# Optimization experiments

Hardware: AMD Instinct MI355X
Metric: run time of the kernel (lower is better)

## Reference

```python
import jax, jax.numpy as jnp
import numpy as np

B = 128          # batch of codewords
M_CHK = 288      # n_check_nodes
N_VAR = 576      # n_variable_nodes
K_INFO = 288     # n_information_bits
N_ITER = 5
EDGE_P = 0.02    # ~11-12 edges per check row, LDPC-like sparsity


def setup_inputs() -> dict:
    key = jax.random.key(0)
    k1, k2, k3, k4 = jax.random.split(key, 4)
    inputs = jax.random.normal(k1, (B, N_VAR), dtype=jnp.float32)
    # sparse binary parity-check matrix, batched (keras RNN constants carry batch dim)
    H = jax.random.bernoulli(k2, EDGE_P, (B, M_CHK, N_VAR)).astype(jnp.float32)
    sigma2 = 0.5 + 0.5 * jax.random.uniform(k3, (B, 1), dtype=jnp.float32)
    # learned parameters
    input_ponderation = jnp.ones((N_ITER, 1), dtype=jnp.float32)
    out_ponderation = jnp.ones((N_ITER, 1), dtype=jnp.float32)
    skip_ponderation = jnp.ones((1, 1), dtype=jnp.float32)
    # per-edge check-to-variable weights of the neural BP cell
    w_cv = 1.0 + 0.02 * jax.random.normal(k4, (M_CHK, N_VAR), dtype=jnp.float32)
    gate_logit = jnp.asarray(0.0, dtype=jnp.float32)
    return {"inputs": inputs, "H": H, "sigma2": sigma2,
            "input_ponderation": input_ponderation,
            "out_ponderation": out_ponderation,
            "skip_ponderation": skip_ponderation,
            "w_cv": w_cv, "gate_logit": gate_logit}


def _decode(inputs, H, sigma2, input_ponderation, out_ponderation,
            skip_ponderation, w_cv, gate_logit):
    llrs = -4.0 * inputs / sigma2                                    # [B, n]
    # trainable=True path: normalize by mean |llr|
    norm_llrs = llrs / jnp.mean(jnp.abs(llrs), axis=-1, keepdims=True)
    # tile over iterations and apply input ponderation -> [B, T, n]
    x = norm_llrs[:, None, :] * input_ponderation

    mask = H                                                         # [B, m, n]
    gate = jax.nn.sigmoid(gate_logit)

    def cell(Mstate, x_t):
        # variable-to-check extrinsic messages on edges
        S = jnp.sum(Mstate, axis=1, keepdims=True)                   # [B, 1, n]
        V = (x_t[:, None, :] + S - Mstate) * mask                    # [B, m, n]
        # tanh-product check-node update (product excluding self via divide)
        t = jnp.tanh(0.5 * jnp.clip(V, -15.0, 15.0))
        t_edge = jnp.where(mask > 0, t, 1.0)
        P = jnp.prod(t_edge, axis=-1, keepdims=True)                 # [B, m, 1]
        t_safe = jnp.where(jnp.abs(t_edge) < 1e-7,
                           jnp.where(t_edge >= 0, 1e-7, -1e-7), t_edge)
        r = jnp.clip(P / t_safe, -1.0 + 1e-6, 1.0 - 1e-6)
        M_new = 2.0 * jnp.arctanh(r) * w_cv * mask                   # weighted c2v
        # gated (damped) state update
        M_out = gate * M_new + (1.0 - gate) * Mstate
        posterior = x_t + jnp.sum(M_out, axis=1)                     # [B, n]
        return M_out, posterior

    M0 = jnp.zeros_like(H)
    xs = jnp.swapaxes(x, 0, 1)                                       # [T, B, n]
    _, posts = jax.lax.scan(cell, M0, xs)
    outputs = jnp.swapaxes(posts, 0, 1)                              # [B, T, n]

    # post-normalization per iteration, weighted pooling over iterations
    norm_out = outputs / jnp.mean(jnp.abs(outputs), axis=-1, keepdims=True)
    pooled = jnp.mean(out_ponderation * norm_out, axis=-2)           # [B, n]
    out = pooled + skip_ponderation * norm_llrs                      # [1,1] broadcast
    return jax.nn.sigmoid(-out[:, :K_INFO])


def reference(inputs, H, sigma2, input_ponderation, out_ponderation,
              skip_ponderation, w_cv, gate_logit):
    return _decode(inputs, H, sigma2, input_ponderation, out_ponderation,
                   skip_ponderation, w_cv, gate_logit)
```

## Files before the change

kernel.cpp:

```cpp
#include <hip/hip_runtime.h>
#include <hip/hip_bf16.h>

#define B_SZ 128
#define MCHK 288
#define NVAR 576
#define KINFO 288
#define NITER 5
#define CAP 40
#define LCAP 3712
#define TPB 1024

__global__ __launch_bounds__(256) void build_edges(const float* __restrict__ H,
                                                   int* __restrict__ cntG,
                                                   unsigned short* __restrict__ idxG) {
    int row  = blockIdx.x * 4 + (threadIdx.x >> 6);
    int lane = threadIdx.x & 63;
    const float* hrow = H + (size_t)row * NVAR;
    const float4* h4  = (const float4*)hrow;
    float4 a = h4[lane];
    float4 bq = h4[64 + lane];
    float  c = hrow[512 + lane];
    int cnt = (a.x!=0.f)+(a.y!=0.f)+(a.z!=0.f)+(a.w!=0.f)
            + (bq.x!=0.f)+(bq.y!=0.f)+(bq.z!=0.f)+(bq.w!=0.f) + (c!=0.f);
    int pre = cnt;
    #pragma unroll
    for (int o = 1; o < 64; o <<= 1) {
        int n = __shfl_up(pre, o, 64);
        if (lane >= o) pre += n;
    }
    int p = pre - cnt;
    unsigned short* dst = idxG + (size_t)row * CAP;
    int base = lane * 4;
    if (a.x!=0.f)  { if (p<CAP) dst[p] = (unsigned short)(base    ); p++; }
    if (a.y!=0.f)  { if (p<CAP) dst[p] = (unsigned short)(base + 1); p++; }
    if (a.z!=0.f)  { if (p<CAP) dst[p] = (unsigned short)(base + 2); p++; }
    if (a.w!=0.f)  { if (p<CAP) dst[p] = (unsigned short)(base + 3); p++; }
    if (bq.x!=0.f) { if (p<CAP) dst[p] = (unsigned short)(256 + base    ); p++; }
    if (bq.y!=0.f) { if (p<CAP) dst[p] = (unsigned short)(256 + base + 1); p++; }
    if (bq.z!=0.f) { if (p<CAP) dst[p] = (unsigned short)(256 + base + 2); p++; }
    if (bq.w!=0.f) { if (p<CAP) dst[p] = (unsigned short)(256 + base + 3); p++; }
    if (c!=0.f)    { if (p<CAP) dst[p] = (unsigned short)(512 + lane);     p++; }
    if (lane == 63) cntG[row] = (pre > CAP) ? CAP : pre;
}

__global__ __launch_bounds__(TPB) void decode(
    const float* __restrict__ inp,   const float* __restrict__ sigma2,
    const float* __restrict__ ipond, const float* __restrict__ opond,
    const float* __restrict__ skipp, const float* __restrict__ wcv,
    const float* __restrict__ gatel, const int* __restrict__ cntG,
    const unsigned short* __restrict__ idxG, float* __restrict__ out) {

    __shared__ float xln[NVAR];
    __shared__ float S[NVAR];
    __shared__ float pooled[NVAR];
    __shared__ float Prow[MCHK];
    __shared__ float Mld[LCAP];
    __shared__ float tld[LCAP];
    __shared__ unsigned int ev[LCAP];
    __shared__ int   rcnt[MCHK];
    __shared__ int   roff[MCHK];
    __shared__ float red[16];
    __shared__ float scal;
    __shared__ int   EtotS;

    const int b    = blockIdx.x;
    const int tid  = threadIdx.x;
    const int wid  = tid >> 6;
    const int lane = tid & 63;

    const float sig  = sigma2[b];
    const float gate = 1.0f / (1.0f + __expf(-gatel[0]));
    const float gbar = 1.0f - gate;
    const float skip = skipp[0];

    float l = 0.0f, al = 0.0f;
    if (tid < NVAR) { l = -4.0f * inp[(size_t)b * NVAR + tid] / sig; al = fabsf(l); }
    #pragma unroll
    for (int o = 32; o; o >>= 1) al += __shfl_down(al, o, 64);
    if (lane == 0) red[wid] = al;

    int* sc = (int*)tld;
    if (tid < 512) {
        int cc = 0;
        if (tid < MCHK) { cc = cntG[b * MCHK + tid]; rcnt[tid] = cc; }
        sc[tid] = cc;
    }
    __syncthreads();
    if (tid == 0) {
        float s = 0.0f;
        #pragma unroll
        for (int i = 0; i < 16; ++i) s += red[i];
        scal = (float)NVAR / s;
    }
    __syncthreads();
    if (tid < NVAR) {
        xln[tid]    = l * scal;
        pooled[tid] = 0.0f;
        S[tid]      = 0.0f;
    }
    for (int d = 1; d < 512; d <<= 1) {
        int v = 0;
        if (tid < 512) v = sc[tid] + ((tid >= d) ? sc[tid - d] : 0);
        __syncthreads();
        if (tid < 512) sc[tid] = v;
        __syncthreads();
    }
    if (tid < MCHK) {
        int c = rcnt[tid];
        int o = sc[tid] - c;
        if (o >= LCAP)            { o = 0; c = 0; }
        else if (o + c > LCAP)    { c = LCAP - o; }
        roff[tid] = o; rcnt[tid] = c;
        const unsigned short* ig = idxG + ((size_t)b * MCHK + tid) * CAP;
        for (int j = 0; j < c; ++j) {
            int v = ig[j];
            ev[o + j]  = ((unsigned)tid << 16) | (unsigned)v;
            Mld[o + j] = 0.0f;
        }
    }
    if (tid == 0) EtotS = (sc[MCHK - 1] > LCAP) ? LCAP : sc[MCHK - 1];
    __syncthreads();
    const int E = EtotS;

    float ipl[NITER], opl[NITER];
    #pragma unroll
    for (int t = 0; t < NITER; ++t) { ipl[t] = ipond[t]; opl[t] = opond[t]; }

    for (int t = 0; t < NITER; ++t) {
        const float pt = ipl[t], ot = opl[t];

        for (int e = tid; e < E; e += TPB) {
            int v   = (int)(ev[e] & 0xFFFFu);
            float V = fmaf(pt, xln[v], S[v]) - Mld[e];
            V = fminf(15.0f, fmaxf(-15.0f, V));
            float ex = __expf(V);
            float te = (ex - 1.0f) * __builtin_amdgcn_rcpf(ex + 1.0f);
            float x  = 0.5f * V, x2 = x * x;
            float tp = x * fmaf(x2, fmaf(x2, fmaf(x2, -0.05396825f, 0.13333333f),
                                         -0.33333333f), 1.0f);
            tld[e] = (fabsf(V) < 0.5f) ? tp : te;
        }
        __syncthreads();

        if (tid < MCHK) {
            int c = rcnt[tid], o = roff[tid];
            float P = 1.0f;
            for (int j = 0; j < c; ++j) P *= tld[o + j];
            Prow[tid] = P;
        }
        if (tid < NVAR) S[tid] = 0.0f;
        __syncthreads();

        for (int e = tid; e < E; e += TPB) {
            unsigned pk = ev[e];
            int v = (int)(pk & 0xFFFFu);
            int m = (int)(pk >> 16);
            float tj = tld[e];
            float ts = (fabsf(tj) < 1e-7f) ? ((tj >= 0.0f) ? 1e-7f : -1e-7f) : tj;
            float r  = Prow[m] * __builtin_amdgcn_rcpf(ts);
            r = fminf(1.0f - 1e-6f, fmaxf(-1.0f + 1e-6f, r));
            float w  = wcv[m * NVAR + v];
            float Mn = __logf((1.0f + r) * __builtin_amdgcn_rcpf(1.0f - r)) * w;
            float Mo = fmaf(gate, Mn, gbar * Mld[e]);
            Mld[e] = Mo;
            atomicAdd(&S[v], Mo);
        }
        __syncthreads();

        float post = 0.0f, ap = 0.0f;
        if (tid < NVAR) { post = fmaf(pt, xln[tid], S[tid]); ap = fabsf(post); }
        #pragma unroll
        for (int o = 32; o; o >>= 1) ap += __shfl_down(ap, o, 64);
        if (lane == 0) red[wid] = ap;
        __syncthreads();
        if (tid == 0) {
            float s2 = 0.0f;
            #pragma unroll
            for (int i = 0; i < 16; ++i) s2 += red[i];
            scal = (float)NVAR / s2;
        }
        __syncthreads();
        if (tid < NVAR) pooled[tid] += ot * post * scal;
    }

    if (tid < KINFO) {
        float o = pooled[tid] * (1.0f / NITER) + skip * xln[tid];
        out[(size_t)b * KINFO + tid] = 1.0f / (1.0f + __expf(o));
    }
}

extern "C" void kernel_launch(void* const* d_in, const int* in_sizes, int n_in,
                              void* d_out, int out_size, void* d_ws, size_t ws_size,
                              hipStream_t stream) {
    const float* inp    = (const float*)d_in[0];
    const float* H      = (const float*)d_in[1];
    const float* sigma2 = (const float*)d_in[2];
    const float* ipond  = (const float*)d_in[3];
    const float* opond  = (const float*)d_in[4];
    const float* skipp  = (const float*)d_in[5];
    const float* wcv    = (const float*)d_in[6];
    const float* gatel  = (const float*)d_in[7];
    float* out = (float*)d_out;

    int* cntG = (int*)d_ws;
    unsigned short* idxG =
        (unsigned short*)((char*)d_ws + (size_t)B_SZ * MCHK * sizeof(int));

    build_edges<<<(B_SZ * MCHK) / 4, 256, 0, stream>>>(H, cntG, idxG);
    decode<<<B_SZ, TPB, 0, stream>>>(inp, sigma2, ipond, opond, skipp,
                                     wcv, gatel, cntG, idxG, out);
}
```

Measured before the change: 173.7 us.

## Fuse edge-list construction into decode kernel with shared-memory staging

Removes the separate build_edges kernel and has each decode block scan its own batch's H rows, staging per-row edge indices in shared memory that is aliased onto the message/tanh buffers. The block-wide Hillis-Steele row-offset scan with many barriers is replaced by a wave-level shuffle scan plus a small cross-wave sum. This drops one launch and the global round trip of the index lists. In exchange, each of the 128 blocks now streams its 663 KB of H itself, so only 128 blocks share the H read bandwidth instead of many small blocks.

```diff
diff --git a/kernel.cpp b/kernel.cpp
--- a/kernel.cpp
+++ b/kernel.cpp
@@ -1,5 +1,4 @@
 #include <hip/hip_runtime.h>
-#include <hip/hip_bf16.h>
 
 #define B_SZ 128
 #define MCHK 288
@@ -10,58 +9,29 @@
 #define LCAP 3712
 #define TPB 1024
 
-__global__ __launch_bounds__(256) void build_edges(const float* __restrict__ H,
-                                                   int* __restrict__ cntG,
-                                                   unsigned short* __restrict__ idxG) {
-    int row  = blockIdx.x * 4 + (threadIdx.x >> 6);
-    int lane = threadIdx.x & 63;
-    const float* hrow = H + (size_t)row * NVAR;
-    const float4* h4  = (const float4*)hrow;
-    float4 a = h4[lane];
-    float4 bq = h4[64 + lane];
-    float  c = hrow[512 + lane];
-    int cnt = (a.x!=0.f)+(a.y!=0.f)+(a.z!=0.f)+(a.w!=0.f)
-            + (bq.x!=0.f)+(bq.y!=0.f)+(bq.z!=0.f)+(bq.w!=0.f) + (c!=0.f);
-    int pre = cnt;
-    #pragma unroll
-    for (int o = 1; o < 64; o <<= 1) {
-        int n = __shfl_up(pre, o, 64);
-        if (lane >= o) pre += n;
-    }
-    int p = pre - cnt;
-    unsigned short* dst = idxG + (size_t)row * CAP;
-    int base = lane * 4;
-    if (a.x!=0.f)  { if (p<CAP) dst[p] = (unsigned short)(base    ); p++; }
-    if (a.y!=0.f)  { if (p<CAP) dst[p] = (unsigned short)(base + 1); p++; }
-    if (a.z!=0.f)  { if (p<CAP) dst[p] = (unsigned short)(base + 2); p++; }
-    if (a.w!=0.f)  { if (p<CAP) dst[p] = (unsigned short)(base + 3); p++; }
-    if (bq.x!=0.f) { if (p<CAP) dst[p] = (unsigned short)(256 + base    ); p++; }
-    if (bq.y!=0.f) { if (p<CAP) dst[p] = (unsigned short)(256 + base + 1); p++; }
-    if (bq.z!=0.f) { if (p<CAP) dst[p] = (unsigned short)(256 + base + 2); p++; }
-    if (bq.w!=0.f) { if (p<CAP) dst[p] = (unsigned short)(256 + base + 3); p++; }
-    if (c!=0.f)    { if (p<CAP) dst[p] = (unsigned short)(512 + lane);     p++; }
-    if (lane == 63) cntG[row] = (pre > CAP) ? CAP : pre;
-}
-
 __global__ __launch_bounds__(TPB) void decode(
-    const float* __restrict__ inp,   const float* __restrict__ sigma2,
+    const float* __restrict__ inp,   const float* __restrict__ H,
+    const float* __restrict__ sigma2,
     const float* __restrict__ ipond, const float* __restrict__ opond,
     const float* __restrict__ skipp, const float* __restrict__ wcv,
-    const float* __restrict__ gatel, const int* __restrict__ cntG,
-    const unsigned short* __restrict__ idxG, float* __restrict__ out) {
-
+    const float* __restrict__ gatel, float* __restrict__ out) {
+
+    __shared__ __align__(16) float MT[2 * LCAP];
+    __shared__ unsigned int ev[LCAP];
     __shared__ float xln[NVAR];
     __shared__ float S[NVAR];
     __shared__ float pooled[NVAR];
     __shared__ float Prow[MCHK];
-    __shared__ float Mld[LCAP];
-    __shared__ float tld[LCAP];
-    __shared__ unsigned int ev[LCAP];
     __shared__ int   rcnt[MCHK];
     __shared__ int   roff[MCHK];
     __shared__ float red[16];
+    __shared__ int   wsumI[16];
     __shared__ float scal;
     __shared__ int   EtotS;
+
+    float* const Mld = MT;
+    float* const tld = MT + LCAP;
+    unsigned short* const stage = (unsigned short*)MT;
 
     const int b    = blockIdx.x;
     const int tid  = threadIdx.x;
@@ -73,18 +43,77 @@
     const float gbar = 1.0f - gate;
     const float skip = skipp[0];
 
-    float l = 0.0f, al = 0.0f;
-    if (tid < NVAR) { l = -4.0f * inp[(size_t)b * NVAR + tid] / sig; al = fabsf(l); }
+    float l = 0.0f;
+    if (tid < NVAR) l = -4.0f * inp[(size_t)b * NVAR + tid] / sig;
+
+    const float* Hb = H + (size_t)b * (MCHK * NVAR);
+    for (int m = wid; m < MCHK; m += 16) {
+        const float* hrow = Hb + (size_t)m * NVAR;
+        const float4* h4  = (const float4*)hrow;
+        float4 a  = h4[lane];
+        float4 bq = h4[64 + lane];
+        float  c  = hrow[512 + lane];
+        int cnt = (a.x!=0.f)+(a.y!=0.f)+(a.z!=0.f)+(a.w!=0.f)
+                + (bq.x!=0.f)+(bq.y!=0.f)+(bq.z!=0.f)+(bq.w!=0.f) + (c!=0.f);
+        int pre = cnt;
+        #pragma unroll
+        for (int o = 1; o < 64; o <<= 1) {
+            int n = __shfl_up(pre, o, 64);
+            if (lane >= o) pre += n;
+        }
+        int p = pre - cnt;
+        unsigned short* dst = stage + m * CAP;
+        int base = lane * 4;
+        if (a.x!=0.f)  { if (p<CAP) dst[p] = (unsigned short)(base    ); p++; }
+        if (a.y!=0.f)  { if (p<CAP) dst[p] = (unsigned short)(base + 1); p++; }
+        if (a.z!=0.f)  { if (p<CAP) dst[p] = (unsigned short)(base + 2); p++; }
+        if (a.w!=0.f)  { if (p<CAP) dst[p] = (unsigned short)(base + 3); p++; }
+        if (bq.x!=0.f) { if (p<CAP) dst[p] = (unsigned short)(256 + base    ); p++; }
+        if (bq.y!=0.f) { if (p<CAP) dst[p] = (unsigned short)(256 + base + 1); p++; }
+        if (bq.z!=0.f) { if (p<CAP) dst[p] = (unsigned short)(256 + base + 2); p++; }
+        if (bq.w!=0.f) { if (p<CAP) dst[p] = (unsigned short)(256 + base + 3); p++; }
+        if (c!=0.f)    { if (p<CAP) dst[p] = (unsigned short)(512 + lane);     p++; }
+        if (lane == 63) rcnt[m] = (pre > CAP) ? CAP : pre;
+    }
+    __syncthreads();
+
+    int myc = 0, incl = 0;
+    if (tid < 320) {
+        myc  = (tid < MCHK) ? rcnt[tid] : 0;
+        incl = myc;
+        #pragma unroll
+        for (int o = 1; o < 64; o <<= 1) {
+            int n = __shfl_up(incl, o, 64);
+            if (lane >= o) incl += n;
+        }
+        if (lane == 63) wsumI[wid] = incl;
+    }
+    __syncthreads();
+    if (tid < MCHK) {
+        int o = incl - myc;
+        #pragma unroll
+        for (int w = 0; w < 4; ++w) if (w < wid) o += wsumI[w];
+        int c = myc;
+        if (o >= LCAP)         { o = 0; c = 0; }
+        else if (o + c > LCAP) { c = LCAP - o; }
+        roff[tid] = o; rcnt[tid] = c;
+        const unsigned short* sg = stage + tid * CAP;
+        for (int j = 0; j < c; ++j)
+            ev[o + j] = ((unsigned)tid << 16) | (unsigned)sg[j];
+    }
+    if (tid == 0) {
+        int e = wsumI[0] + wsumI[1] + wsumI[2] + wsumI[3] + wsumI[4];
+        EtotS = (e > LCAP) ? LCAP : e;
+    }
+    __syncthreads();
+    const int E = EtotS;
+
+    float al = (tid < NVAR) ? fabsf(l) : 0.0f;
     #pragma unroll
     for (int o = 32; o; o >>= 1) al += __shfl_down(al, o, 64);
     if (lane == 0) red[wid] = al;
-
-    int* sc = (int*)tld;
-    if (tid < 512) {
-        int cc = 0;
-        if (tid < MCHK) { cc = cntG[b * MCHK + tid]; rcnt[tid] = cc; }
-        sc[tid] = cc;
-    }
+    for (int e = tid; e < E; e += TPB) Mld[e] = 0.0f;
+    if (tid < NVAR) { S[tid] = 0.0f; pooled[tid] = 0.0f; }
     __syncthreads();
     if (tid == 0) {
         float s = 0.0f;
@@ -93,34 +122,8 @@
         scal = (float)NVAR / s;
     }
     __syncthreads();
-    if (tid < NVAR) {
-        xln[tid]    = l * scal;
-        pooled[tid] = 0.0f;
-        S[tid]      = 0.0f;
-    }
-    for (int d = 1; d < 512; d <<= 1) {
-        int v = 0;
-        if (tid < 512) v = sc[tid] + ((tid >= d) ? sc[tid - d] : 0);
-        __syncthreads();
-        if (tid < 512) sc[tid] = v;
-        __syncthreads();
-    }
-    if (tid < MCHK) {
-        int c = rcnt[tid];
-        int o = sc[tid] - c;
-        if (o >= LCAP)            { o = 0; c = 0; }
-        else if (o + c > LCAP)    { c = LCAP - o; }
-        roff[tid] = o; rcnt[tid] = c;
-        const unsigned short* ig = idxG + ((size_t)b * MCHK + tid) * CAP;
-        for (int j = 0; j < c; ++j) {
-            int v = ig[j];
-            ev[o + j]  = ((unsigned)tid << 16) | (unsigned)v;
-            Mld[o + j] = 0.0f;
-        }
-    }
-    if (tid == 0) EtotS = (sc[MCHK - 1] > LCAP) ? LCAP : sc[MCHK - 1];
-    __syncthreads();
-    const int E = EtotS;
+    if (tid < NVAR) xln[tid] = l * scal;
+    __syncthreads();
 
     float ipl[NITER], opl[NITER];
     #pragma unroll
@@ -202,11 +205,6 @@
     const float* gatel  = (const float*)d_in[7];
     float* out = (float*)d_out;
 
-    int* cntG = (int*)d_ws;
-    unsigned short* idxG =
-        (unsigned short*)((char*)d_ws + (size_t)B_SZ * MCHK * sizeof(int));
-
-    build_edges<<<(B_SZ * MCHK) / 4, 256, 0, stream>>>(H, cntG, idxG);
-    decode<<<B_SZ, TPB, 0, stream>>>(inp, sigma2, ipond, opond, skipp,
-                                     wcv, gatel, cntG, idxG, out);
+    decode<<<B_SZ, TPB, 0, stream>>>(inp, H, sigma2, ipond, opond, skipp,
+                                     wcv, gatel, out);
 }
```

Measured after the change: 177.2 us. +2.0%, slower.
